# Kernel optimization log

Hardware: AMD Instinct MI355X
Metric: run time of the kernel (lower is better)

Reference implementation:

```python
import jax, jax.numpy as jnp
import numpy as np

# Dimensions (match init_kwargs / input_specs)
B, C, H, W = 16, 16, 64, 64
N = H * W          # num_nodes
D_E = 64           # node_embed_dim
D_H = 128          # gnn_hidden_dim
D_R = 256          # readout_output_dim


def _param(key, shape, fan_in):
    return jax.random.normal(key, shape, jnp.float32) * (1.0 / np.sqrt(fan_in))


def setup_inputs() -> dict:
    key = jax.random.key(0)
    ks = jax.random.split(key, 16)
    inp = {
        "obs": jax.random.normal(ks[0], (B, C, H, W), jnp.float32),
        # node_embedding MLP (2 layers: C -> D_E -> D_E)
        "e1_w": _param(ks[1], (C, D_E), C),   "e1_b": jnp.zeros((D_E,), jnp.float32),
        "e2_w": _param(ks[2], (D_E, D_E), D_E), "e2_b": jnp.zeros((D_E,), jnp.float32),
        # 3 GNN layers (Linear then adjacency aggregation)
        "g1_w": _param(ks[3], (D_E, D_H), D_E), "g1_b": jnp.zeros((D_H,), jnp.float32),
        "g2_w": _param(ks[4], (D_H, D_H), D_H), "g2_b": jnp.zeros((D_H,), jnp.float32),
        "g3_w": _param(ks[5], (D_H, D_H), D_H), "g3_b": jnp.zeros((D_H,), jnp.float32),
        # readout MLP (2 layers: D_H -> 2*D_H -> D_R)
        "r1_w": _param(ks[6], (D_H, 2 * D_H), D_H),   "r1_b": jnp.zeros((2 * D_H,), jnp.float32),
        "r2_w": _param(ks[7], (2 * D_H, D_R), 2 * D_H), "r2_b": jnp.zeros((D_R,), jnp.float32),
    }
    return inp


def _adj_norm():
    # 4-neighbor grid adjacency on an H x W grid, row-normalized (same for every
    # batch element, so build once as (N, N) instead of (B, N, N)).
    idx = jnp.arange(N)
    up = jnp.eye(N, k=-W, dtype=jnp.float32)                      # i > 0
    down = jnp.eye(N, k=W, dtype=jnp.float32)                     # i < H-1
    left = jnp.eye(N, k=-1, dtype=jnp.float32) * ((idx % W) != 0)[:, None]
    right = jnp.eye(N, k=1, dtype=jnp.float32) * ((idx % W) != (W - 1))[:, None]
    adj = up + down + left + right
    return adj / (adj.sum(axis=1, keepdims=True) + 1e-6)


def reference(obs, e1_w, e1_b, e2_w, e2_b,
              g1_w, g1_b, g2_w, g2_b, g3_w, g3_b,
              r1_w, r1_b, r2_w, r2_b):
    relu = jax.nn.relu
    # grid -> graph: (B, C, H, W) -> (B, N, C)
    x = jnp.transpose(obs, (0, 2, 3, 1)).reshape(B, N, C)
    # node embedding MLP (output activation per ding MLP default)
    h = relu(x @ e1_w + e1_b)
    h = relu(h @ e2_w + e2_b)
    A = _adj_norm()  # (N, N)
    for Wg, bg in ((g1_w, g1_b), (g2_w, g2_b), (g3_w, g3_b)):
        support = h @ Wg + bg                      # (B, N, D_H)
        h = relu(jnp.einsum('nm,bmf->bnf', A, support))
    g = h.mean(axis=1)                              # (B, D_H) graph readout
    g = relu(g @ r1_w + r1_b)
    return relu(g @ r2_w + r2_b)                    # (B, D_R)
```

## Files before the change

kernel.cpp:

```cpp
#include <hip/hip_runtime.h>


typedef __attribute__((ext_vector_type(8))) short bf16x8;
typedef __attribute__((ext_vector_type(4))) float f32x4;
#define MFMA(a, b, c) __builtin_amdgcn_mfma_f32_16x16x32_bf16(a, b, c, 0, 0, 0)

__device__ inline void block_sync_lgkm() {
    asm volatile("" ::: "memory");
    __builtin_amdgcn_s_waitcnt(0xC07F);
    __builtin_amdgcn_s_barrier();
    asm volatile("" ::: "memory");
}

__device__ inline ushort bf16h(float x) {
    unsigned u = __float_as_uint(x);
    return (ushort)((u + 0x7fffu + ((u >> 16) & 1u)) >> 16);
}
__device__ inline void split_bf16(float x, ushort& hi, ushort& lo) {
    hi = bf16h(x);
    lo = bf16h(x - __uint_as_float(((unsigned)hi) << 16));
}
__device__ inline unsigned pack_split(float x) {
    unsigned u = __float_as_uint(x);
    unsigned hi = (u + 0x7fffu + ((u >> 16) & 1u)) >> 16;
    float r = x - __uint_as_float(hi << 16);
    return (hi << 16) | (__float_as_uint(r) >> 16);
}
__device__ inline void frag_packed(const unsigned* bp, bf16x8& bh, bf16x8& bl) {
    unsigned p[8];
#pragma unroll
    for (int j = 0; j < 8; j++) p[j] = bp[j * 65];
    union { bf16x8 v; unsigned d[4]; } H, L;
#pragma unroll
    for (int j = 0; j < 4; j++) {
        const unsigned e = p[2 * j], o = p[2 * j + 1];
        H.d[j] = (o & 0xFFFF0000u) | (e >> 16);
        L.d[j] = (o << 16) | (e & 0xFFFFu);
    }
    bh = H.v; bl = L.v;
}

__global__ __launch_bounds__(256, 4) void prep_embed_kernel(
    const float* __restrict__ obs,
    const float* __restrict__ e1w, const float* __restrict__ e1b,
    const float* __restrict__ e2w, const float* __restrict__ e2b,
    const float* __restrict__ g1w, const float* __restrict__ g2w,
    const float* __restrict__ g3w, ushort* __restrict__ wf,
    float* __restrict__ gsum, float* __restrict__ h0)
{
    const int blk = blockIdx.x, tid = threadIdx.x;

    if (blk < 20) {
        const int u = blk * 4 + (tid >> 6);
        const int l = tid & 63;
        const float* src; int K, kc, t; ushort* dst;
        if (u < 16)      { src = g1w; K = 64;  kc = u >> 3;        t = u & 7; dst = wf + 12288; }
        else if (u < 48) { src = g2w; K = 128; kc = (u - 16) >> 3; t = (u - 16) & 7; dst = wf + 28672; }
        else             { src = g3w; K = 128; kc = (u - 48) >> 3; t = (u - 48) & 7; dst = wf + 61440; }
        ushort* uh = dst + ((kc * 8 + t) * 2 + 0) * 512 + l * 8;
        ushort* ul = dst + ((kc * 8 + t) * 2 + 1) * 512 + l * 8;
        const int fw = t * 16 + (l & 15);
        const int kb = kc * 32 + ((l >> 4) << 3);
#pragma unroll
        for (int j = 0; j < 8; j++) {
            const int k = kb + j;
            const float wv = (k < K) ? src[k * 128 + fw] : 0.f;
            ushort hi, lo; split_bf16(wv, hi, lo);
            uh[j] = hi; ul[j] = lo;
        }
    } else if (blk < 28) {
        gsum[(blk - 20) * 256 + tid] = 0.f;
    }

    __shared__ unsigned lds[6240];
    const int ebid = ((blk & 7) << 7) | (blk >> 3);
    const int b = ebid >> 6, row = ebid & 63;
    const int lane = tid & 63, w = tid >> 6, quad = lane >> 4, nl = lane & 15;
    const int cp = tid >> 4, nq = tid & 15;

    const float4 x4 = *(const float4*)(obs + ((size_t)(b * 16 + cp) << 12) + row * 64 + nq * 4);

    float e1f[8], e2f[16];
    {
        const int f = 16 * w + nl;
#pragma unroll
        for (int j = 0; j < 8; j++) {
            const int k = quad * 8 + j;
            e1f[j] = (k < 16) ? e1w[k * 64 + f] : 0.f;
        }
#pragma unroll
        for (int kc = 0; kc < 2; kc++)
#pragma unroll
            for (int j = 0; j < 8; j++)
                e2f[kc * 8 + j] = e2w[(kc * 32 + quad * 8 + j) * 64 + f];
    }

    unsigned* Xs = lds;
    unsigned* Hs = lds + 2080;
    {
        unsigned* xp = Xs + cp * 65 + nq * 4;
        xp[0] = pack_split(x4.x); xp[1] = pack_split(x4.y);
        xp[2] = pack_split(x4.z); xp[3] = pack_split(x4.w);
        unsigned* zp = Xs + (16 + cp) * 65 + nq * 4;
        zp[0] = 0u; zp[1] = 0u; zp[2] = 0u; zp[3] = 0u;
    }

    bf16x8 e1h, e1l, e2h[2], e2l[2];
#pragma unroll
    for (int j = 0; j < 8; j++) {
        ushort hi, lo; split_bf16(e1f[j], hi, lo);
        e1h[j] = (short)hi; e1l[j] = (short)lo;
    }
#pragma unroll
    for (int kc = 0; kc < 2; kc++)
#pragma unroll
        for (int j = 0; j < 8; j++) {
            ushort hi, lo; split_bf16(e2f[kc * 8 + j], hi, lo);
            e2h[kc][j] = (short)hi; e2l[kc][j] = (short)lo;
        }
    __syncthreads();

#pragma unroll
    for (int nt = 0; nt < 4; nt++) {
        const unsigned* bp = Xs + (quad * 8) * 65 + nt * 16 + nl;
        bf16x8 bh, bl; frag_packed(bp, bh, bl);
        f32x4 c = {0.f, 0.f, 0.f, 0.f};
        c = MFMA(e1h, bh, c); c = MFMA(e1h, bl, c); c = MFMA(e1l, bh, c);
#pragma unroll
        for (int reg = 0; reg < 4; reg++) {
            const int fm = 16 * w + quad * 4 + reg;
            Hs[fm * 65 + nt * 16 + nl] = pack_split(fmaxf(c[reg] + e1b[fm], 0.f));
        }
    }
    __syncthreads();

    f32x4 a2[4];
#pragma unroll
    for (int nt = 0; nt < 4; nt++) a2[nt] = (f32x4){0.f, 0.f, 0.f, 0.f};
#pragma unroll
    for (int kc = 0; kc < 2; kc++) {
#pragma unroll
        for (int nt = 0; nt < 4; nt++) {
            const unsigned* bp = Hs + (kc * 32 + quad * 8) * 65 + nt * 16 + nl;
            bf16x8 bh, bl; frag_packed(bp, bh, bl);
            a2[nt] = MFMA(e2h[kc], bh, a2[nt]);
            a2[nt] = MFMA(e2h[kc], bl, a2[nt]);
            a2[nt] = MFMA(e2l[kc], bh, a2[nt]);
        }
    }
#pragma unroll
    for (int reg = 0; reg < 4; reg++) {
        const int f = 16 * w + quad * 4 + reg;
        const float bv = e2b[f];
#pragma unroll
        for (int nt = 0; nt < 4; nt++)
            h0[((size_t)(b * 64 + f) << 12) + row * 64 + nt * 16 + nl] =
                fmaxf(a2[nt][reg] + bv, 0.f);
    }
}

template <int K, bool MEAN>
__global__ __launch_bounds__(256, 4) void gnn_kernel(
    const float* __restrict__ hin, const ushort* __restrict__ wf,
    const float* __restrict__ bias, float* __restrict__ hout,
    float* __restrict__ gsum)
{
    constexpr int NQ = K / 32;
    __shared__ unsigned As[2][32 * 65];
    const int tid = threadIdx.x;
    const int bid = ((blockIdx.x & 7) << 7) | (blockIdx.x >> 3);
    const int b = bid >> 6, row = bid & 63;
    const int lane = tid & 63, w = tid >> 6, quad = lane >> 4, nl = lane & 15;
    const int kp = tid >> 4, nq = tid & 15;
    const float* hb = hin + (size_t)b * K * 4096;
    const int rowu = (row > 0) ? row - 1 : row;
    const int rowd = (row < 63) ? row + 1 : row;
    const float su = (row > 0) ? 1.f : 0.f;
    const float sd = (row < 63) ? 1.f : 0.f;
    float inv[4];
#pragma unroll
    for (int i = 0; i < 4; i++) {
        const int n = nq * 4 + i;
        const int deg = (row > 0) + (row < 63) + (n > 0) + (n < 63);
        inv[i] = 1.f / ((float)deg + 1e-6f);
    }

    const ushort* wfl = wf + lane * 8;
    f32x4 acc[4][2];
#pragma unroll
    for (int nt = 0; nt < 4; nt++) {
        acc[nt][0] = (f32x4){0.f, 0.f, 0.f, 0.f};
        acc[nt][1] = (f32x4){0.f, 0.f, 0.f, 0.f};
    }

    float4 S[6];
    bf16x8 V[2][2];

    auto sload = [&](int q) {
#pragma unroll
        for (int it = 0; it < 2; it++) {
            const int kg = q * 32 + it * 16 + kp;
            const float* pk = hb + ((size_t)kg << 12) + nq * 4;
            S[it * 3 + 0] = *(const float4*)(pk + row * 64);
            S[it * 3 + 1] = *(const float4*)(pk + rowu * 64);
            S[it * 3 + 2] = *(const float4*)(pk + rowd * 64);
        }
    };
    auto wload = [&](int q) {
#pragma unroll
        for (int ftl = 0; ftl < 2; ftl++) {
            V[ftl][0] = *(const bf16x8*)(wfl + ((q * 8 + 2 * w + ftl) * 2) * 512);
            V[ftl][1] = *(const bf16x8*)(wfl + ((q * 8 + 2 * w + ftl) * 2 + 1) * 512);
        }
    };
    auto stage = [&](unsigned* Ab) {
#pragma unroll
        for (int it = 0; it < 2; it++) {
            const int kl = it * 16 + kp;
            const float4 c4 = S[it * 3 + 0];
            const float4 u4 = S[it * 3 + 1];
            const float4 d4 = S[it * 3 + 2];
            const float pw = __shfl_up(c4.w, 1);
            const float nx = __shfl_down(c4.x, 1);
            const float lx = (nq > 0) ? pw : 0.f;
            const float rw = (nq < 15) ? nx : 0.f;
            unsigned* ap = Ab + kl * 65 + nq * 4;
            ap[0] = pack_split((su * u4.x + sd * d4.x + lx + c4.y) * inv[0]);
            ap[1] = pack_split((su * u4.y + sd * d4.y + c4.x + c4.z) * inv[1]);
            ap[2] = pack_split((su * u4.z + sd * d4.z + c4.y + c4.w) * inv[2]);
            ap[3] = pack_split((su * u4.w + sd * d4.w + c4.z + rw) * inv[3]);
        }
    };
    auto consume = [&](const unsigned* Ab) {
#pragma unroll
        for (int nt = 0; nt < 4; nt++) {
            const unsigned* bp = Ab + (quad * 8) * 65 + nt * 16 + nl;
            bf16x8 bh, bl; frag_packed(bp, bh, bl);
            acc[nt][0] = MFMA(V[0][0], bh, acc[nt][0]);
            acc[nt][0] = MFMA(V[0][0], bl, acc[nt][0]);
            acc[nt][0] = MFMA(V[0][1], bh, acc[nt][0]);
            acc[nt][1] = MFMA(V[1][0], bh, acc[nt][1]);
            acc[nt][1] = MFMA(V[1][0], bl, acc[nt][1]);
            acc[nt][1] = MFMA(V[1][1], bh, acc[nt][1]);
        }
    };

    wload(0);
    sload(0);
    stage(As[0]);
    sload(1);
    block_sync_lgkm();

#pragma unroll
    for (int q = 0; q < NQ; q++) {
        consume(As[q & 1]);
        if (q + 1 < NQ) {
            wload(q + 1);
            stage(As[(q + 1) & 1]);
            if (q + 2 < NQ) sload(q + 2);
            block_sync_lgkm();
        }
    }

    if (!MEAN) {
#pragma unroll
        for (int ftl = 0; ftl < 2; ftl++) {
            const int fb = 32 * w + 16 * ftl + quad * 4;
            const float b0 = bias[fb], b1 = bias[fb + 1], b2 = bias[fb + 2], b3 = bias[fb + 3];
#pragma unroll
            for (int nt = 0; nt < 4; nt++) {
                const int n = 16 * nt + nl;
                const int deg = (row > 0) + (row < 63) + (n > 0) + (n < 63);
                const float rs = (float)deg / ((float)deg + 1e-6f);
                float* op = hout + ((size_t)(b * 128 + fb) << 12) + row * 64 + n;
                op[0]        = fmaxf(acc[nt][ftl][0] + rs * b0, 0.f);
                op[1u << 12] = fmaxf(acc[nt][ftl][1] + rs * b1, 0.f);
                op[2u << 12] = fmaxf(acc[nt][ftl][2] + rs * b2, 0.f);
                op[3u << 12] = fmaxf(acc[nt][ftl][3] + rs * b3, 0.f);
            }
        }
    } else {
#pragma unroll
        for (int ftl = 0; ftl < 2; ftl++) {
            const int fb = 32 * w + 16 * ftl + quad * 4;
#pragma unroll
            for (int reg = 0; reg < 4; reg++) {
                const float bv = bias[fb + reg];
                float v = 0.f;
#pragma unroll
                for (int nt = 0; nt < 4; nt++) {
                    const int n = 16 * nt + nl;
                    const int deg = (row > 0) + (row < 63) + (n > 0) + (n < 63);
                    const float rs = (float)deg / ((float)deg + 1e-6f);
                    v += fmaxf(acc[nt][ftl][reg] + rs * bv, 0.f);
                }
                v += __shfl_xor(v, 1); v += __shfl_xor(v, 2);
                v += __shfl_xor(v, 4); v += __shfl_xor(v, 8);
                if (nl == 0) atomicAdd(&gsum[b * 128 + fb + reg], v * (1.f / 4096.f));
            }
        }
    }
}

__global__ __launch_bounds__(256) void readout_kernel(
    const float* __restrict__ gsum, const float* __restrict__ r1w,
    const float* __restrict__ r1b, const float* __restrict__ r2w,
    const float* __restrict__ r2b, float* __restrict__ out)
{
    __shared__ float gs[128];
    __shared__ float g2[256];
    const int b = blockIdx.x, tid = threadIdx.x;
    if (tid < 128) gs[tid] = gsum[b * 128 + tid];
    __syncthreads();
    float a = r1b[tid];
#pragma unroll 16
    for (int k = 0; k < 128; k++) a = fmaf(gs[k], r1w[k * 256 + tid], a);
    g2[tid] = fmaxf(a, 0.f);
    __syncthreads();
    float a2 = r2b[tid];
#pragma unroll 16
    for (int k = 0; k < 256; k++) a2 = fmaf(g2[k], r2w[k * 256 + tid], a2);
    out[b * 256 + tid] = fmaxf(a2, 0.f);
}

extern "C" void kernel_launch(void* const* d_in, const int* in_sizes, int n_in,
                              void* d_out, int out_size, void* d_ws, size_t ws_size,
                              hipStream_t stream)
{
    const float* obs = (const float*)d_in[0];
    const float* e1w = (const float*)d_in[1];
    const float* e1b = (const float*)d_in[2];
    const float* e2w = (const float*)d_in[3];
    const float* e2b = (const float*)d_in[4];
    const float* g1w = (const float*)d_in[5];
    const float* g1b = (const float*)d_in[6];
    const float* g2w = (const float*)d_in[7];
    const float* g2b = (const float*)d_in[8];
    const float* g3w = (const float*)d_in[9];
    const float* g3b = (const float*)d_in[10];
    const float* r1w = (const float*)d_in[11];
    const float* r1b = (const float*)d_in[12];
    const float* r2w = (const float*)d_in[13];
    const float* r2b = (const float*)d_in[14];
    float* out = (float*)d_out;
    float* ws = (float*)d_ws;

    float* h0 = ws;
    float* h1 = ws + 4194304;
    float* h2 = ws + 4194304 + 8388608;
    float* gsum = (float*)((char*)d_ws + 80u * 1024u * 1024u);
    ushort* wfb = (ushort*)((char*)d_ws + 80u * 1024u * 1024u + 8192u);

    hipLaunchKernelGGL(prep_embed_kernel, dim3(1024), dim3(256), 0, stream,
                       obs, e1w, e1b, e2w, e2b, g1w, g2w, g3w, wfb, gsum, h0);
    hipLaunchKernelGGL((gnn_kernel<64, false>), dim3(1024), dim3(256), 0, stream,
                       h0, wfb + 12288, g1b, h1, nullptr);
    hipLaunchKernelGGL((gnn_kernel<128, false>), dim3(1024), dim3(256), 0, stream,
                       h1, wfb + 28672, g2b, h2, nullptr);
    hipLaunchKernelGGL((gnn_kernel<128, true>), dim3(1024), dim3(256), 0, stream,
                       h2, wfb + 61440, g3b, nullptr, gsum);
    hipLaunchKernelGGL(readout_kernel, dim3(16), dim3(256), 0, stream,
                       gsum, r1w, r1b, r2w, r2b, out);
}
```

Baseline: 159.6 us.

## Store intermediate GNN activations in bf16 to halve memory traffic

Intermediate node features between the embedding and GNN layers are written and read as bf16 instead of fp32. The staging code is rewritten so each thread loads 8 packed bf16 values and unpacks them for the stencil aggregation. The prefetch schedule is also deepened to two stages ahead. This reduces the HBM bandwidth of the memory-bound layers but loses precision in the stored activations compared with the previous split-bf16 near-fp32 path.

```diff
diff --git a/kernel.cpp b/kernel.cpp
--- a/kernel.cpp
+++ b/kernel.cpp
@@ -26,6 +26,8 @@
     float r = x - __uint_as_float(hi << 16);
     return (hi << 16) | (__float_as_uint(r) >> 16);
 }
+__device__ inline float bflo(unsigned w) { return __uint_as_float(w << 16); }
+__device__ inline float bfhi(unsigned w) { return __uint_as_float(w & 0xFFFF0000u); }
 __device__ inline void frag_packed(const unsigned* bp, bf16x8& bh, bf16x8& bl) {
     unsigned p[8];
 #pragma unroll
@@ -46,7 +48,7 @@
     const float* __restrict__ e2w, const float* __restrict__ e2b,
     const float* __restrict__ g1w, const float* __restrict__ g2w,
     const float* __restrict__ g3w, ushort* __restrict__ wf,
-    float* __restrict__ gsum, float* __restrict__ h0)
+    float* __restrict__ gsum, ushort* __restrict__ h0)
 {
     const int blk = blockIdx.x, tid = threadIdx.x;
 
@@ -155,14 +157,14 @@
 #pragma unroll
         for (int nt = 0; nt < 4; nt++)
             h0[((size_t)(b * 64 + f) << 12) + row * 64 + nt * 16 + nl] =
-                fmaxf(a2[nt][reg] + bv, 0.f);
+                bf16h(fmaxf(a2[nt][reg] + bv, 0.f));
     }
 }
 
 template <int K, bool MEAN>
 __global__ __launch_bounds__(256, 4) void gnn_kernel(
-    const float* __restrict__ hin, const ushort* __restrict__ wf,
-    const float* __restrict__ bias, float* __restrict__ hout,
+    const ushort* __restrict__ hin, const ushort* __restrict__ wf,
+    const float* __restrict__ bias, ushort* __restrict__ hout,
     float* __restrict__ gsum)
 {
     constexpr int NQ = K / 32;
@@ -171,18 +173,18 @@
     const int bid = ((blockIdx.x & 7) << 7) | (blockIdx.x >> 3);
     const int b = bid >> 6, row = bid & 63;
     const int lane = tid & 63, w = tid >> 6, quad = lane >> 4, nl = lane & 15;
-    const int kp = tid >> 4, nq = tid & 15;
-    const float* hb = hin + (size_t)b * K * 4096;
+    const int kp8 = tid >> 3, nq8 = tid & 7;
+    const ushort* hb = hin + (size_t)b * K * 4096;
     const int rowu = (row > 0) ? row - 1 : row;
     const int rowd = (row < 63) ? row + 1 : row;
     const float su = (row > 0) ? 1.f : 0.f;
     const float sd = (row < 63) ? 1.f : 0.f;
-    float inv[4];
-#pragma unroll
-    for (int i = 0; i < 4; i++) {
-        const int n = nq * 4 + i;
+    float inv8[8];
+#pragma unroll
+    for (int i = 0; i < 8; i++) {
+        const int n = nq8 * 8 + i;
         const int deg = (row > 0) + (row < 63) + (n > 0) + (n < 63);
-        inv[i] = 1.f / ((float)deg + 1e-6f);
+        inv8[i] = 1.f / ((float)deg + 1e-6f);
     }
 
     const ushort* wfl = wf + lane * 8;
@@ -196,15 +198,12 @@
     float4 S[6];
     bf16x8 V[2][2];
 
-    auto sload = [&](int q) {
-#pragma unroll
-        for (int it = 0; it < 2; it++) {
-            const int kg = q * 32 + it * 16 + kp;
-            const float* pk = hb + ((size_t)kg << 12) + nq * 4;
-            S[it * 3 + 0] = *(const float4*)(pk + row * 64);
-            S[it * 3 + 1] = *(const float4*)(pk + rowu * 64);
-            S[it * 3 + 2] = *(const float4*)(pk + rowd * 64);
-        }
+    auto sload = [&](int q, int s) {
+        const int kg = q * 32 + kp8;
+        const ushort* pk = hb + ((size_t)kg << 12) + nq8 * 8;
+        S[s * 3 + 0] = *(const float4*)(pk + row * 64);
+        S[s * 3 + 1] = *(const float4*)(pk + rowu * 64);
+        S[s * 3 + 2] = *(const float4*)(pk + rowd * 64);
     };
     auto wload = [&](int q) {
 #pragma unroll
@@ -213,22 +212,30 @@
             V[ftl][1] = *(const bf16x8*)(wfl + ((q * 8 + 2 * w + ftl) * 2 + 1) * 512);
         }
     };
-    auto stage = [&](unsigned* Ab) {
-#pragma unroll
-        for (int it = 0; it < 2; it++) {
-            const int kl = it * 16 + kp;
-            const float4 c4 = S[it * 3 + 0];
-            const float4 u4 = S[it * 3 + 1];
-            const float4 d4 = S[it * 3 + 2];
-            const float pw = __shfl_up(c4.w, 1);
-            const float nx = __shfl_down(c4.x, 1);
-            const float lx = (nq > 0) ? pw : 0.f;
-            const float rw = (nq < 15) ? nx : 0.f;
-            unsigned* ap = Ab + kl * 65 + nq * 4;
-            ap[0] = pack_split((su * u4.x + sd * d4.x + lx + c4.y) * inv[0]);
-            ap[1] = pack_split((su * u4.y + sd * d4.y + c4.x + c4.z) * inv[1]);
-            ap[2] = pack_split((su * u4.z + sd * d4.z + c4.y + c4.w) * inv[2]);
-            ap[3] = pack_split((su * u4.w + sd * d4.w + c4.z + rw) * inv[3]);
+    auto stage = [&](unsigned* Ab, int s) {
+        const float4 c4 = S[s * 3 + 0];
+        const float4 u4 = S[s * 3 + 1];
+        const float4 d4 = S[s * 3 + 2];
+        const unsigned cw[4] = {__float_as_uint(c4.x), __float_as_uint(c4.y),
+                                __float_as_uint(c4.z), __float_as_uint(c4.w)};
+        const unsigned uw[4] = {__float_as_uint(u4.x), __float_as_uint(u4.y),
+                                __float_as_uint(u4.z), __float_as_uint(u4.w)};
+        const unsigned dw[4] = {__float_as_uint(d4.x), __float_as_uint(d4.y),
+                                __float_as_uint(d4.z), __float_as_uint(d4.w)};
+        const unsigned pw = __shfl_up(cw[3], 1);
+        const unsigned nx = __shfl_down(cw[0], 1);
+        unsigned* ap = Ab + kp8 * 65 + nq8 * 8;
+        float cl = (nq8 > 0) ? bfhi(pw) : 0.f;
+#pragma unroll
+        for (int j = 0; j < 4; j++) {
+            const float ce = bflo(cw[j]), co = bfhi(cw[j]);
+            const float ue = bflo(uw[j]), uo = bfhi(uw[j]);
+            const float de = bflo(dw[j]), dd = bfhi(dw[j]);
+            const float ro = (j < 3) ? bflo(cw[j + 1])
+                                     : ((nq8 < 7) ? bflo(nx) : 0.f);
+            ap[2 * j]     = pack_split((su * ue + sd * de + cl + co) * inv8[2 * j]);
+            ap[2 * j + 1] = pack_split((su * uo + sd * dd + ce + ro) * inv8[2 * j + 1]);
+            cl = co;
         }
     };
     auto consume = [&](const unsigned* Ab) {
@@ -246,9 +253,10 @@
     };
 
     wload(0);
-    sload(0);
-    stage(As[0]);
-    sload(1);
+    sload(0, 0);
+    if (NQ > 1) sload(1, 1);
+    stage(As[0], 0);
+    if (NQ > 2) sload(2, 0);
     block_sync_lgkm();
 
 #pragma unroll
@@ -256,8 +264,8 @@
         consume(As[q & 1]);
         if (q + 1 < NQ) {
             wload(q + 1);
-            stage(As[(q + 1) & 1]);
-            if (q + 2 < NQ) sload(q + 2);
+            stage(As[(q + 1) & 1], (q + 1) & 1);
+            if (q + 3 < NQ) sload(q + 3, (q + 3) & 1);
             block_sync_lgkm();
         }
     }
@@ -272,11 +280,11 @@
                 const int n = 16 * nt + nl;
                 const int deg = (row > 0) + (row < 63) + (n > 0) + (n < 63);
                 const float rs = (float)deg / ((float)deg + 1e-6f);
-                float* op = hout + ((size_t)(b * 128 + fb) << 12) + row * 64 + n;
-                op[0]        = fmaxf(acc[nt][ftl][0] + rs * b0, 0.f);
-                op[1u << 12] = fmaxf(acc[nt][ftl][1] + rs * b1, 0.f);
-                op[2u << 12] = fmaxf(acc[nt][ftl][2] + rs * b2, 0.f);
-                op[3u << 12] = fmaxf(acc[nt][ftl][3] + rs * b3, 0.f);
+                ushort* op = hout + ((size_t)(b * 128 + fb) << 12) + row * 64 + n;
+                op[0]        = bf16h(fmaxf(acc[nt][ftl][0] + rs * b0, 0.f));
+                op[1u << 12] = bf16h(fmaxf(acc[nt][ftl][1] + rs * b1, 0.f));
+                op[2u << 12] = bf16h(fmaxf(acc[nt][ftl][2] + rs * b2, 0.f));
+                op[3u << 12] = bf16h(fmaxf(acc[nt][ftl][3] + rs * b3, 0.f));
             }
         }
     } else {
@@ -343,13 +351,12 @@
     const float* r2w = (const float*)d_in[13];
     const float* r2b = (const float*)d_in[14];
     float* out = (float*)d_out;
-    float* ws = (float*)d_ws;
-
-    float* h0 = ws;
-    float* h1 = ws + 4194304;
-    float* h2 = ws + 4194304 + 8388608;
-    float* gsum = (float*)((char*)d_ws + 80u * 1024u * 1024u);
-    ushort* wfb = (ushort*)((char*)d_ws + 80u * 1024u * 1024u + 8192u);
+
+    ushort* h0 = (ushort*)d_ws;
+    ushort* h1 = (ushort*)((char*)d_ws + (16u << 20));
+    ushort* h2 = (ushort*)((char*)d_ws + (48u << 20));
+    float* gsum = (float*)((char*)d_ws + (80u << 20));
+    ushort* wfb = (ushort*)((char*)d_ws + (80u << 20) + 8192u);
 
     hipLaunchKernelGGL(prep_embed_kernel, dim3(1024), dim3(256), 0, stream,
                        obs, e1w, e1b, e2w, e2b, g1w, g2w, g3w, wfb, gsum, h0);
```

After: 149.8 us. 6.1% less time.
